# Optimization experiments

Hardware: AMD Instinct MI355X
Metric: run time of the kernel (lower is better)

The kernel has to match this reference:

```python
import jax, jax.numpy as jnp
import numpy as np

L_MAX = 2    # l in {0,1,2}, m-dim sizes 2l+1
NU_MAX = 3   # body order
K = 8        # number of CG m-combinations kept per l_tuple
Q = 16       # radial channels
S = 256      # atomic environments (samples)


def _build_structure():
    """Deterministically build combine_indices + multiplicities (module state).
    Returns {nu: [(l_tuple, idx_prev[K], idx_1[K], mult[K]), ...]} in sorted order."""
    rng = np.random.default_rng(0)
    struct = {}
    # nu = 2: l_tuples are nondecreasing pairs; previous level is LE_1 with m-dim 2*l1+1
    struct[2] = []
    for l1 in range(L_MAX + 1):
        for l2 in range(l1, L_MAX + 1):
            ip = jnp.asarray(rng.integers(0, 2 * l1 + 1, K), dtype=jnp.int32)
            i1 = jnp.asarray(rng.integers(0, 2 * l2 + 1, K), dtype=jnp.int32)
            mult = jnp.asarray((rng.random(K) + 0.5).astype(np.float32))
            struct[2].append(((l1, l2), ip, i1, mult))
    # nu = 3: previous level tensors have m-dim K
    struct[3] = []
    for l1 in range(L_MAX + 1):
        for l2 in range(l1, L_MAX + 1):
            for l3 in range(l2, L_MAX + 1):
                ip = jnp.asarray(rng.integers(0, K, K), dtype=jnp.int32)
                i1 = jnp.asarray(rng.integers(0, 2 * l3 + 1, K), dtype=jnp.int32)
                mult = jnp.asarray((rng.random(K) + 0.5).astype(np.float32))
                struct[3].append(((l1, l2, l3), ip, i1, mult))
    return struct


def setup_inputs() -> dict:
    key = jax.random.key(0)
    k0, k1, k2 = jax.random.split(key, 3)
    return {
        "LE1_l0": jax.random.normal(k0, (1, Q, S), dtype=jnp.float32),
        "LE1_l1": jax.random.normal(k1, (3, Q, S), dtype=jnp.float32),
        "LE1_l2": jax.random.normal(k2, (5, Q, S), dtype=jnp.float32),
    }


def reference(LE1_l0, LE1_l1, LE1_l2):
    struct = _build_structure()
    LE1 = {(0,): LE1_l0, (1,): LE1_l1, (2,): LE1_l2}
    feats = {1: LE1}
    # Build all levels from UNSCALED parents (multiplicities applied afterwards,
    # matching the torch loop order exactly).
    for nu in range(2, NU_MAX + 1):
        cur = {}
        for lt, ip, i1, _ in struct[nu]:
            A = jnp.take(feats[nu - 1][lt[:-1]], ip, axis=0)[:, :, None, :]  # [K, F, 1, S]
            B = jnp.take(LE1[(lt[-1],)], i1, axis=0)[:, None, :, :]          # [K, 1, Q, S]
            cur[lt] = (A * B).reshape(K, -1, S)                               # [K, F*Q, S]
        feats[nu] = cur
    # Apply multiplicities, then flatten everything into one [total_rows, S] output
    outs = []
    for nu in range(2, NU_MAX + 1):
        for lt, _, _, mult in struct[nu]:
            outs.append((feats[nu][lt] * mult[:, None, None]).reshape(-1, S))
    return jnp.concatenate(outs, axis=0)
```

## Files before the change

kernel.cpp:

```cpp
#include <hip/hip_runtime.h>
#include <stdint.h>
#include <stddef.h>

#define KK 8
#define QQ 16
#define SS 256
#define NU2_ROWS 12288u
#define NUNITS 21248u
#define NWAVES 2048u

typedef float f32x4 __attribute__((ext_vector_type(4)));

namespace {

struct NpPcg64 {
  unsigned __int128 state, inc;
  uint32_t uinteger;
  bool has_uint32;

  static unsigned __int128 mul128() {
    return (((unsigned __int128)2549297995355413924ULL) << 64) | 4865540595714422341ULL;
  }
  void step() { state = state * mul128() + inc; }
  uint64_t next64() {
    step();
    uint64_t hi = (uint64_t)(state >> 64), lo = (uint64_t)state;
    uint64_t x = hi ^ lo;
    unsigned rot = (unsigned)(state >> 122) & 63u;
    return (x >> rot) | (x << ((64u - rot) & 63u));
  }
  uint32_t next32() {
    if (has_uint32) { has_uint32 = false; return uinteger; }
    uint64_t n = next64();
    has_uint32 = true;
    uinteger = (uint32_t)(n >> 32);
    return (uint32_t)n;
  }
  double nextd() {
    return (double)(next64() >> 11) * (1.0 / 9007199254740992.0);
  }
  uint32_t lemire32(uint32_t rng) {
    uint32_t excl = rng + 1u;
    uint64_t m = (uint64_t)next32() * (uint64_t)excl;
    uint32_t leftover = (uint32_t)m;
    if (leftover < excl) {
      uint32_t threshold = (uint32_t)((0xFFFFFFFFu - rng) % excl);
      while (leftover < threshold) {
        m = (uint64_t)next32() * (uint64_t)excl;
        leftover = (uint32_t)m;
      }
    }
    return (uint32_t)(m >> 32);
  }
  void integers(int high, int* out, int n) {
    if (high <= 1) { for (int i = 0; i < n; i++) out[i] = 0; return; }
    uint32_t rng = (uint32_t)(high - 1);
    for (int i = 0; i < n; i++) out[i] = (int)lemire32(rng);
  }
  void mults(float* out, int n) {
    for (int i = 0; i < n; i++) out[i] = (float)(nextd() + 0.5);
  }
};

void seed_rng0(NpPcg64& r) {
  uint32_t pool[4];
  uint32_t hc = 0x43b0d7e5u;
  auto hashmix = [&hc](uint32_t v) -> uint32_t {
    v ^= hc; hc *= 0x931e8875u; v *= hc; v ^= v >> 16; return v;
  };
  auto mix = [](uint32_t x, uint32_t y) -> uint32_t {
    uint32_t m = 0xca01f9ddu * x - 0x4973f715u * y; m ^= m >> 16; return m;
  };
  for (int i = 0; i < 4; i++) pool[i] = hashmix(0u);
  for (int is = 0; is < 4; is++)
    for (int id = 0; id < 4; id++)
      if (is != id) pool[id] = mix(pool[id], hashmix(pool[is]));
  uint32_t hb = 0x8b51f9ddu;
  uint32_t w[8];
  for (int i = 0; i < 8; i++) {
    uint32_t v = pool[i & 3];
    v ^= hb; hb *= 0x58f38dedu; v *= hb; v ^= v >> 16;
    w[i] = v;
  }
  uint64_t sd[4];
  for (int i = 0; i < 4; i++) sd[i] = (uint64_t)w[2 * i] | ((uint64_t)w[2 * i + 1] << 32);
  unsigned __int128 initstate = (((unsigned __int128)sd[0]) << 64) | sd[1];
  unsigned __int128 initseq   = (((unsigned __int128)sd[2]) << 64) | sd[3];
  r.state = 0; r.inc = (initseq << 1) | 1;
  r.step(); r.state += initstate; r.step();
  r.has_uint32 = false; r.uinteger = 0;
}

struct Args {
  const float* pA2[6][KK];
  const float* pB2[6][KK];
  float        m2[6][KK];
  const float* pX3[10][KK];
  const float* pY3[10][KK];
  const float* pZ3[10][KK];
  float        m3[10][KK];
};

}

__global__ __launch_bounds__(256) void le_kernel(Args a, float* __restrict__ out) {
  unsigned gwave = (blockIdx.x * 256u + threadIdx.x) >> 6;
  unsigned s4 = (threadIdx.x & 63u) << 2;

  for (unsigned w = gwave; w < NUNITS; w += NWAVES) {
    if (w < 768u) {
      unsigned t = w >> 7, k = (w >> 4) & 7u, q1 = w & 15u;
      const f32x4 va = *(const f32x4*)(a.pA2[t][k] + q1 * SS + s4);
      const float* pb = a.pB2[t][k] + s4;
      float m = a.m2[t][k];
      float* po = out + (size_t)((t * 8u + k) * 16u + q1) * 16u * SS + s4;
#pragma unroll
      for (unsigned q2 = 0; q2 < 16u; ++q2) {
        f32x4 vb = *(const f32x4*)(pb + q2 * SS);
        f32x4 r = (va * vb) * m;
        *(f32x4*)(po + q2 * SS) = r;
      }
    } else {
      unsigned u = w - 768u;
      unsigned t = u >> 11, k = (u >> 8) & 7u, q1 = (u >> 4) & 15u, q2 = u & 15u;
      const f32x4 vx = *(const f32x4*)(a.pX3[t][k] + q1 * SS + s4);
      const f32x4 vy = *(const f32x4*)(a.pY3[t][k] + q2 * SS + s4);
      const float* pz = a.pZ3[t][k] + s4;
      float m = a.m3[t][k];
      f32x4 xy = vx * vy;
      float* po = out +
          (size_t)(NU2_ROWS + (((t * 8u + k) * 16u + q1) * 16u + q2) * 16u) * SS + s4;
#pragma unroll
      for (unsigned q3 = 0; q3 < 16u; ++q3) {
        f32x4 vz = *(const f32x4*)(pz + q3 * SS);
        f32x4 r = (xy * vz) * m;
        *(f32x4*)(po + q3 * SS) = r;
      }
    }
  }
}

extern "C" void kernel_launch(void* const* d_in, const int* in_sizes, int n_in,
                              void* d_out, int out_size, void* d_ws, size_t ws_size,
                              hipStream_t stream) {
  (void)in_sizes; (void)n_in; (void)d_ws; (void)ws_size; (void)out_size;

  NpPcg64 rng;
  seed_rng0(rng);

  static const int pairs[6][2] = {{0,0},{0,1},{0,2},{1,1},{1,2},{2,2}};
  static const int trip[10][3] = {{0,0,0},{0,0,1},{0,0,2},{0,1,1},{0,1,2},
                                  {0,2,2},{1,1,1},{1,1,2},{1,2,2},{2,2,2}};
  static const int parent[10]  = {0,0,0,1,1,2,3,3,4,5};

  int   ip2[6][KK], i12[6][KK];
  float m2v[6][KK];
  for (int t = 0; t < 6; t++) {
    rng.integers(2 * pairs[t][0] + 1, ip2[t], KK);
    rng.integers(2 * pairs[t][1] + 1, i12[t], KK);
    rng.mults(m2v[t], KK);
  }
  int   ip3[10][KK], i13[10][KK];
  float m3v[10][KK];
  for (int u = 0; u < 10; u++) {
    rng.integers(KK, ip3[u], KK);
    rng.integers(2 * trip[u][2] + 1, i13[u], KK);
    rng.mults(m3v[u], KK);
  }

  const float* base[3] = {(const float*)d_in[0], (const float*)d_in[1], (const float*)d_in[2]};
  Args a;
  for (int t = 0; t < 6; t++) {
    for (int k = 0; k < KK; k++) {
      a.pA2[t][k] = base[pairs[t][0]] + (size_t)ip2[t][k] * QQ * SS;
      a.pB2[t][k] = base[pairs[t][1]] + (size_t)i12[t][k] * QQ * SS;
      a.m2[t][k]  = m2v[t][k];
    }
  }
  for (int u = 0; u < 10; u++) {
    for (int k = 0; k < KK; k++) {
      int p = parent[u], kp = ip3[u][k];
      a.pX3[u][k] = base[pairs[p][0]] + (size_t)ip2[p][kp] * QQ * SS;
      a.pY3[u][k] = base[pairs[p][1]] + (size_t)i12[p][kp] * QQ * SS;
      a.pZ3[u][k] = base[trip[u][2]] + (size_t)i13[u][k] * QQ * SS;
      a.m3[u][k]  = m3v[u][k];
    }
  }

  unsigned blocks = NWAVES * 64u / 256u;
  le_kernel<<<blocks, 256, 0, stream>>>(a, (float*)d_out);
}
```

Before: 68.43 us.

## Assign one wave per (t,k,q1) unit and cache Y/Z rows in registers

Restructures the work split so each wave handles a whole (t,k,q1) block: nu=3 waves preload 16 Y and 16 Z vectors into registers and emit all 256 q2×q3 rows, while nu=2 waves handle their 16 rows. The grid-stride loop and per-unit index decoding are removed and the grid is fixed at 512 blocks. This cuts redundant input loads and address math, but concentrates work in fewer, longer-running waves and raises register pressure.

Measured after the change: 71.83 us. 1.05x slower.

```diff
diff --git a/kernel.cpp b/kernel.cpp
--- a/kernel.cpp
+++ b/kernel.cpp
@@ -6,8 +6,6 @@
 #define QQ 16
 #define SS 256
 #define NU2_ROWS 12288u
-#define NUNITS 21248u
-#define NWAVES 2048u
 
 typedef float f32x4 __attribute__((ext_vector_type(4)));
 
@@ -107,35 +105,40 @@
   unsigned gwave = (blockIdx.x * 256u + threadIdx.x) >> 6;
   unsigned s4 = (threadIdx.x & 63u) << 2;
 
-  for (unsigned w = gwave; w < NUNITS; w += NWAVES) {
-    if (w < 768u) {
-      unsigned t = w >> 7, k = (w >> 4) & 7u, q1 = w & 15u;
-      const f32x4 va = *(const f32x4*)(a.pA2[t][k] + q1 * SS + s4);
-      const float* pb = a.pB2[t][k] + s4;
-      float m = a.m2[t][k];
-      float* po = out + (size_t)((t * 8u + k) * 16u + q1) * 16u * SS + s4;
+  if (gwave < 1280u) {
+    unsigned t = gwave >> 7, k = (gwave >> 4) & 7u, q1 = gwave & 15u;
+    const f32x4 vx = *(const f32x4*)(a.pX3[t][k] + q1 * SS + s4);
+    const float* py = a.pY3[t][k] + s4;
+    const float* pz = a.pZ3[t][k] + s4;
+    f32x4 vy[16], vz[16];
 #pragma unroll
-      for (unsigned q2 = 0; q2 < 16u; ++q2) {
-        f32x4 vb = *(const f32x4*)(pb + q2 * SS);
-        f32x4 r = (va * vb) * m;
-        *(f32x4*)(po + q2 * SS) = r;
+    for (int i = 0; i < 16; i++) vy[i] = *(const f32x4*)(py + i * SS);
+#pragma unroll
+    for (int i = 0; i < 16; i++) vz[i] = *(const f32x4*)(pz + i * SS);
+    float m = a.m3[t][k];
+    float* po = out + (size_t)(NU2_ROWS + ((t * 8u + k) * 16u + q1) * 256u) * SS + s4;
+#pragma unroll
+    for (int q2 = 0; q2 < 16; q2++) {
+      f32x4 xy = vx * vy[q2];
+      float* pr = po + (size_t)(q2 * 16) * SS;
+#pragma unroll
+      for (int q3 = 0; q3 < 16; q3++) {
+        f32x4 r = (xy * vz[q3]) * m;
+        *(f32x4*)(pr + q3 * SS) = r;
       }
-    } else {
-      unsigned u = w - 768u;
-      unsigned t = u >> 11, k = (u >> 8) & 7u, q1 = (u >> 4) & 15u, q2 = u & 15u;
-      const f32x4 vx = *(const f32x4*)(a.pX3[t][k] + q1 * SS + s4);
-      const f32x4 vy = *(const f32x4*)(a.pY3[t][k] + q2 * SS + s4);
-      const float* pz = a.pZ3[t][k] + s4;
-      float m = a.m3[t][k];
-      f32x4 xy = vx * vy;
-      float* po = out +
-          (size_t)(NU2_ROWS + (((t * 8u + k) * 16u + q1) * 16u + q2) * 16u) * SS + s4;
+    }
+  } else {
+    unsigned u = gwave - 1280u;
+    unsigned t = u >> 7, k = (u >> 4) & 7u, q1 = u & 15u;
+    const f32x4 va = *(const f32x4*)(a.pA2[t][k] + q1 * SS + s4);
+    const float* pb = a.pB2[t][k] + s4;
+    float m = a.m2[t][k];
+    float* po = out + (size_t)((t * 8u + k) * 16u + q1) * 16u * SS + s4;
 #pragma unroll
-      for (unsigned q3 = 0; q3 < 16u; ++q3) {
-        f32x4 vz = *(const f32x4*)(pz + q3 * SS);
-        f32x4 r = (xy * vz) * m;
-        *(f32x4*)(po + q3 * SS) = r;
-      }
+    for (int q2 = 0; q2 < 16; q2++) {
+      f32x4 vb = *(const f32x4*)(pb + q2 * SS);
+      f32x4 r = (va * vb) * m;
+      *(f32x4*)(po + q2 * SS) = r;
     }
   }
 }
@@ -187,6 +190,5 @@
     }
   }
 
-  unsigned blocks = NWAVES * 64u / 256u;
-  le_kernel<<<blocks, 256, 0, stream>>>(a, (float*)d_out);
+  le_kernel<<<512, 256, 0, stream>>>(a, (float*)d_out);
 }
```
